# Kernel optimization log

Hardware: AMD Instinct MI355X
Metric: run time of the kernel (lower is better)

The kernel has to match this reference:

```python
import jax, jax.numpy as jnp
import numpy as np
import math

B, S, INP = 64, 512, 64
D, H, L, DFF, LAT = 512, 8, 2, 2048, 128
SPARSE = 0.1  # sparse_factor default used by TransformerEncoderLayer


def _ln(x, g, b, eps=1e-5):
    m = x.mean(-1, keepdims=True)
    v = ((x - m) ** 2).mean(-1, keepdims=True)
    return (x - m) / jnp.sqrt(v + eps) * g + b


def _pe(s, d):
    pos = jnp.arange(s, dtype=jnp.float32)[:, None]
    div = jnp.exp(jnp.arange(0, d, 2, dtype=jnp.float32) * (-math.log(10000.0) / d))
    pe = jnp.zeros((s, d), dtype=jnp.float32)
    return pe.at[:, 0::2].set(jnp.sin(pos * div)).at[:, 1::2].set(jnp.cos(pos * div))


def _attn(h, g1, b1, wq, wk, wv, woW, wob):
    # h: (S, B, d). Faithful to source: transpose(1,2) yields (S, H, B, dk),
    # so attention is computed ACROSS THE BATCH axis at each timestep.
    s, bb, d = h.shape
    dk = d // H
    res = h
    hn = _ln(h, g1, b1)
    to_heads = lambda w: (hn @ w).reshape(s, bb, H, dk).swapaxes(1, 2)  # (S,H,B,dk)
    q, k, v = to_heads(wq), to_heads(wk), to_heads(wv)
    scores = jnp.einsum('shbd,shcd->shbc', q, k) / math.sqrt(dk)  # (S,H,B,B)
    kk = max(1, int(bb * SPARSE))  # topk row-sparsify before softmax
    thresh = jax.lax.top_k(scores, kk)[0][..., -1:]
    scores = jnp.where(scores >= thresh, scores, -1e9)
    w = jax.nn.softmax(scores, axis=-1)
    ctx = jnp.einsum('shbc,shcd->shbd', w, v).swapaxes(1, 2).reshape(s, bb, d)
    return ctx @ woW + wob + res


def _encoder(x, inW, inb, p):
    # x: (B, S, in_dim) -> (B, S, D)
    h = jnp.swapaxes(x, 0, 1)  # (S, B, in)
    h = (h @ inW + inb) * math.sqrt(D)
    h = h + _pe(h.shape[0], D)[:, None, :]
    for l in range(L):
        h = _attn(h, p['g1'][l], p['b1'][l], p['wq'][l], p['wk'][l], p['wv'][l], p['woW'][l], p['wob'][l])
        res = h
        f = _ln(h, p['g2'][l], p['b2'][l])
        f = jax.nn.gelu(f @ p['f1W'][l] + p['f1b'][l], approximate=False)
        h = f @ p['f2W'][l] + p['f2b'][l] + res
    h = _ln(h, p['gf'], p['bf'])
    return jnp.swapaxes(h, 0, 1)


_PKEYS = ['g1', 'b1', 'wq', 'wk', 'wv', 'woW', 'wob', 'g2', 'b2', 'f1W', 'f1b', 'f2W', 'f2b', 'gf', 'bf']


def _forward(x, enc_in_W, enc_in_b, enc_g1, enc_b1, enc_wq, enc_wk, enc_wv, enc_woW, enc_wob,
             enc_g2, enc_b2, enc_f1W, enc_f1b, enc_f2W, enc_f2b, enc_gf, enc_bf,
             mu_W, mu_b, lv_W, lv_b, dec_in_W, dec_in_b, dec_g1, dec_b1, dec_wq, dec_wk, dec_wv,
             dec_woW, dec_wob, dec_g2, dec_b2, dec_f1W, dec_f1b, dec_f2W, dec_f2b, dec_gf, dec_bf,
             out_W, out_b):
    enc_p = dict(zip(_PKEYS, [enc_g1, enc_b1, enc_wq, enc_wk, enc_wv, enc_woW, enc_wob, enc_g2, enc_b2, enc_f1W, enc_f1b, enc_f2W, enc_f2b, enc_gf, enc_bf]))
    dec_p = dict(zip(_PKEYS, [dec_g1, dec_b1, dec_wq, dec_wk, dec_wv, dec_woW, dec_wob, dec_g2, dec_b2, dec_f1W, dec_f1b, dec_f2W, dec_f2b, dec_gf, dec_bf]))
    enc_out = _encoder(x, enc_in_W, enc_in_b, enc_p)  # (B,S,D)
    pooled = enc_out.mean(axis=1)                      # (B,D)
    mu = pooled @ mu_W + mu_b
    logvar = pooled @ lv_W + lv_b
    z = mu  # eval mode: no reparameterization sampling
    z_seq = jnp.broadcast_to(z[:, None, :], (z.shape[0], S, LAT))
    dec_out = _encoder(z_seq, dec_in_W, dec_in_b, dec_p)
    recon = dec_out @ out_W + out_b
    return recon, mu, logvar


def setup_inputs() -> dict:
    key = jax.random.key(0)
    ks = iter(jax.random.split(key, 64))
    n = lambda shape, s=0.02: jax.random.normal(next(ks), shape, dtype=jnp.float32) * s

    def stack_params():
        return dict(
            g1=jnp.ones((L, D)), b1=jnp.zeros((L, D)),
            wq=n((L, D, D)), wk=n((L, D, D)), wv=n((L, D, D)),
            woW=n((L, D, D)), wob=jnp.zeros((L, D)),
            g2=jnp.ones((L, D)), b2=jnp.zeros((L, D)),
            f1W=n((L, D, DFF)), f1b=jnp.zeros((L, DFF)),
            f2W=n((L, DFF, D)), f2b=jnp.zeros((L, D)),
            gf=jnp.ones((D,)), bf=jnp.zeros((D,)))

    inp = {
        'x': jax.random.normal(next(ks), (B, S, INP), dtype=jnp.float32),
        'enc_in_W': n((INP, D), 0.05), 'enc_in_b': jnp.zeros((D,)),
        'mu_W': n((D, LAT), 0.05), 'mu_b': jnp.zeros((LAT,)),
        'lv_W': n((D, LAT), 0.05), 'lv_b': jnp.zeros((LAT,)),
        'dec_in_W': n((LAT, D), 0.05), 'dec_in_b': jnp.zeros((D,)),
        'out_W': n((D, INP), 0.05), 'out_b': jnp.zeros((INP,)),
    }
    for k_, v in stack_params().items():
        inp['enc_' + k_] = v
    for k_, v in stack_params().items():
        inp['dec_' + k_] = v
    return inp


def reference(x, enc_in_W, enc_in_b, enc_g1, enc_b1, enc_wq, enc_wk, enc_wv, enc_woW, enc_wob,
              enc_g2, enc_b2, enc_f1W, enc_f1b, enc_f2W, enc_f2b, enc_gf, enc_bf,
              mu_W, mu_b, lv_W, lv_b, dec_in_W, dec_in_b, dec_g1, dec_b1, dec_wq, dec_wk, dec_wv,
              dec_woW, dec_wob, dec_g2, dec_b2, dec_f1W, dec_f1b, dec_f2W, dec_f2b, dec_gf, dec_bf,
              out_W, out_b):
    return _forward(x, enc_in_W, enc_in_b, enc_g1, enc_b1, enc_wq, enc_wk, enc_wv, enc_woW, enc_wob,
                    enc_g2, enc_b2, enc_f1W, enc_f1b, enc_f2W, enc_f2b, enc_gf, enc_bf,
                    mu_W, mu_b, lv_W, lv_b, dec_in_W, dec_in_b, dec_g1, dec_b1, dec_wq, dec_wk, dec_wv,
                    dec_woW, dec_wob, dec_g2, dec_b2, dec_f1W, dec_f1b, dec_f2W, dec_f2b, dec_gf, dec_bf,
                    out_W, out_b)
```

## Files before the change

kernel.cpp:

```cpp
#include <hip/hip_runtime.h>
#include <math.h>


#define SQRT_D 22.62741699796952f
#define PE_C   0.017988946039015984f

typedef short frag8 __attribute__((ext_vector_type(8)));
typedef float accf4 __attribute__((ext_vector_type(4)));

#define GLL16(g, l) __builtin_amdgcn_global_load_lds( \
    (const __attribute__((address_space(1))) void*)(g), \
    (__attribute__((address_space(3))) void*)(l), 16, 0, 0)

__device__ __forceinline__ float bf2f(unsigned short u) {
    union { unsigned i; float f; } v; v.i = ((unsigned)u) << 16; return v.f;
}
__device__ __forceinline__ unsigned short f2bf(float f) {
    union { float f; unsigned i; } v; v.f = f;
    unsigned r = v.i + 0x7fff + ((v.i >> 16) & 1);
    return (unsigned short)(r >> 16);
}
__device__ __forceinline__ float pe_val(int s, int d) {
    float div = expf(-(float)(d & ~1) * PE_C);
    float ang = (float)s * div;
    return (d & 1) ? cosf(ang) : sinf(ang);
}
__device__ __forceinline__ float gelu_exact(float x) {
    return 0.5f * x * (1.0f + erff(x * 0.7071067811865476f));
}
__device__ __forceinline__ float gelu_fast(float x) {
    float xs = x * 0.7071067811865476f;
    float ax = fabsf(xs);
    float t  = 1.0f / (1.0f + 0.3275911f * ax);
    float p  = t * (0.254829592f + t * (-0.284496736f + t * (1.421413741f +
               t * (-1.453152027f + t * 1.061405429f))));
    float er = 1.0f - p * __expf(-ax * ax);
    er = (xs < 0.0f) ? -er : er;
    return 0.5f * x * (1.0f + er);
}

__device__ __forceinline__ void phase_bar() {
    __builtin_amdgcn_sched_barrier(0);
    __builtin_amdgcn_s_barrier();
    __builtin_amdgcn_sched_barrier(0);
}

__global__ __launch_bounds__(256) void pe_k(float* __restrict__ pe)
{
    const int s = blockIdx.x;
    const int d = threadIdx.x;
    pe[s * 512 + d]       = pe_val(s, d);
    pe[s * 512 + d + 256] = pe_val(s, d + 256);
}

__global__ __launch_bounds__(256) void embed_gemm_k(
    const float* __restrict__ x, const float* __restrict__ W,
    const float* __restrict__ bias, const float* __restrict__ pe,
    float* __restrict__ h)
{
    __shared__ float As[64][68];
    __shared__ float Ws[64][68];
    const int s = blockIdx.y;
    const int col0 = blockIdx.x * 64;
    const int tid = threadIdx.x;
#pragma unroll
    for (int i = 0; i < 16; i++) {
        int idx = i * 256 + tid;
        int r = idx >> 6, kk = idx & 63;
        As[kk][r] = x[((size_t)r * 512 + s) * 64 + kk];
        Ws[r][kk] = W[(size_t)r * 512 + col0 + kk];
    }
    __syncthreads();
    const int tm = (tid >> 4) << 2;
    const int tn = (tid & 15) << 2;
    float acc[4][4] = {};
#pragma unroll 8
    for (int kk = 0; kk < 64; kk++) {
        float4 a4 = *reinterpret_cast<const float4*>(&As[kk][tm]);
        float4 b4 = *reinterpret_cast<const float4*>(&Ws[kk][tn]);
        const float a[4] = {a4.x, a4.y, a4.z, a4.w};
        const float b[4] = {b4.x, b4.y, b4.z, b4.w};
#pragma unroll
        for (int i = 0; i < 4; i++)
#pragma unroll
            for (int j = 0; j < 4; j++)
                acc[i][j] += a[i] * b[j];
    }
    const int c = col0 + tn;
    float4 bi = *reinterpret_cast<const float4*>(&bias[c]);
    float4 pp = *reinterpret_cast<const float4*>(&pe[s * 512 + c]);
#pragma unroll
    for (int i = 0; i < 4; i++) {
        size_t row = ((size_t)s * 64 + tm + i) * 512;
        float4 o;
        o.x = (acc[i][0] + bi.x) * SQRT_D + pp.x;
        o.y = (acc[i][1] + bi.y) * SQRT_D + pp.y;
        o.z = (acc[i][2] + bi.z) * SQRT_D + pp.z;
        o.w = (acc[i][3] + bi.w) * SQRT_D + pp.w;
        *reinterpret_cast<float4*>(&h[row + c]) = o;
    }
}

__global__ __launch_bounds__(256) void dec_embed_k(
    const float* __restrict__ zemb, const float* __restrict__ pe,
    float* __restrict__ h)
{
    const int i4 = (blockIdx.x * 256 + threadIdx.x) * 4;
    const int d = i4 & 511;
    const int t = i4 >> 9;
    const int s = t >> 6, b = t & 63;
    float4 z = *reinterpret_cast<const float4*>(&zemb[b * 512 + d]);
    float4 p = *reinterpret_cast<const float4*>(&pe[s * 512 + d]);
    float4 o;
    o.x = z.x * SQRT_D + p.x;
    o.y = z.y * SQRT_D + p.y;
    o.z = z.z * SQRT_D + p.z;
    o.w = z.w * SQRT_D + p.w;
    *reinterpret_cast<float4*>(&h[i4]) = o;
}

__global__ __launch_bounds__(256) void stats_k(
    const float* __restrict__ x, float* __restrict__ st)
{
    const int row = blockIdx.x;
    const int tid = threadIdx.x;
    const float* xr = x + (size_t)row * 512;
    float2 vv = *reinterpret_cast<const float2*>(&xr[tid * 2]);
    float v0 = vv.x, v1 = vv.y;
    float ssum = v0 + v1;
#pragma unroll
    for (int off = 32; off > 0; off >>= 1) ssum += __shfl_down(ssum, off, 64);
    __shared__ float red[4];
    __shared__ float red2[4];
    const int wid = tid >> 6, lane = tid & 63;
    if (lane == 0) red[wid] = ssum;
    __syncthreads();
    float m = (red[0] + red[1] + red[2] + red[3]) * (1.f / 512.f);
    float d0 = v0 - m, d1 = v1 - m;
    float s2 = d0 * d0 + d1 * d1;
#pragma unroll
    for (int off = 32; off > 0; off >>= 1) s2 += __shfl_down(s2, off, 64);
    if (lane == 0) red2[wid] = s2;
    __syncthreads();
    if (tid == 0) {
        float var = (red2[0] + red2[1] + red2[2] + red2[3]) * (1.f / 512.f);
        st[row * 2]     = m;
        st[row * 2 + 1] = rsqrtf(var + 1e-5f);
    }
}

__global__ __launch_bounds__(256) void cast_ln_k(
    const float* __restrict__ x, const float* __restrict__ g,
    const float* __restrict__ b, unsigned short* __restrict__ y)
{
    const int row = blockIdx.x;
    const int tid = threadIdx.x;
    const float* xr = x + (size_t)row * 512;
    float2 vv = *reinterpret_cast<const float2*>(&xr[tid * 2]);
    float v0 = vv.x, v1 = vv.y;
    float ssum = v0 + v1;
#pragma unroll
    for (int off = 32; off > 0; off >>= 1) ssum += __shfl_down(ssum, off, 64);
    __shared__ float red[4];
    __shared__ float red2[4];
    const int wid = tid >> 6, lane = tid & 63;
    if (lane == 0) red[wid] = ssum;
    __syncthreads();
    float m = (red[0] + red[1] + red[2] + red[3]) * (1.f / 512.f);
    float d0 = v0 - m, d1 = v1 - m;
    float s2 = d0 * d0 + d1 * d1;
#pragma unroll
    for (int off = 32; off > 0; off >>= 1) s2 += __shfl_down(s2, off, 64);
    if (lane == 0) red2[wid] = s2;
    __syncthreads();
    float var = (red2[0] + red2[1] + red2[2] + red2[3]) * (1.f / 512.f);
    float rstd = rsqrtf(var + 1e-5f);
    float2 gg = *reinterpret_cast<const float2*>(&g[tid * 2]);
    float2 bb = *reinterpret_cast<const float2*>(&b[tid * 2]);
    ushort2 o;
    o.x = f2bf(d0 * rstd * gg.x + bb.x);
    o.y = f2bf(d1 * rstd * gg.y + bb.y);
    *reinterpret_cast<ushort2*>(&y[(size_t)row * 512 + tid * 2]) = o;
}

struct WTDesc { const float* src; unsigned short* dst; int Kd; int Nd; };

__global__ __launch_bounds__(256) void wtcast6_k(
    WTDesc d0, WTDesc d1, WTDesc d2, WTDesc d3, WTDesc d4, WTDesc d5)
{
    WTDesc d;
    switch (blockIdx.z) {
        case 0: d = d0; break; case 1: d = d1; break; case 2: d = d2; break;
        case 3: d = d3; break; case 4: d = d4; break; default: d = d5; break;
    }
    const int n0 = blockIdx.x * 32, k0 = blockIdx.y * 32;
    if (n0 >= d.Nd || k0 >= d.Kd) return;
    __shared__ float t[32][33];
    const int tx = threadIdx.x & 31, ty = threadIdx.x >> 5;
#pragma unroll
    for (int i = 0; i < 32; i += 8)
        t[ty + i][tx] = d.src[(size_t)(k0 + ty + i) * d.Nd + (n0 + tx)];
    __syncthreads();
#pragma unroll
    for (int i = 0; i < 32; i += 8)
        d.dst[(size_t)(n0 + ty + i) * d.Kd + (k0 + tx)] = f2bf(t[tx][ty + i]);
}

template<int ACT, int OUTBF, int RES, int BIAS>
__global__ __launch_bounds__(256, 2) void mgemm128_k(
    const unsigned short* __restrict__ A, int lda,
    const unsigned short* __restrict__ Bt, int ldb,
    const float* __restrict__ bias,
    const float* res, float* Cf, unsigned short* Cb, int ldc, int K)
{
    __shared__ unsigned short sm[32768];
    const int tid = threadIdx.x;
    const int wave = tid >> 6, lane = tid & 63;

    int bx = blockIdx.x, by = blockIdx.y;
    if (gridDim.x == 256) {
        const int id = blockIdx.x + (blockIdx.y << 8);
        const int span = gridDim.y << 4;
        const int xcd = id & 7;
        const int q = id >> 3;
        const int hb = q / span;
        const int r2 = q - hb * span;
        bx = (xcd << 5) + (hb << 4) + (r2 & 15);
        by = r2 >> 4;
    }
    const int row0 = bx * 128;
    const int col0 = by * 128;

    const int wr = wave >> 1, wc = wave & 1;
    const int wrbase = wr * 64, wcbase = wc * 64;
    const int frow = lane & 15;
    const int fcol = (lane >> 4) * 8;
    const int fxorE = (lane & 7) << 3;
    const int ccol = ((lane & 7) ^ (lane >> 3)) * 8;

    const int NT = K >> 6;

    auto stageA = [&](int buf, int k0t) {
#pragma unroll
        for (int i = 0; i < 4; i++) {
            int chunk = wave * 4 + i;
            GLL16(A + (size_t)(row0 + chunk * 8 + (lane >> 3)) * lda + k0t + ccol,
                  &sm[buf * 16384 + chunk * 512]);
        }
    };
    auto stageB = [&](int buf, int k0t) {
#pragma unroll
        for (int i = 0; i < 4; i++) {
            int chunk = wave * 4 + i;
            GLL16(Bt + (size_t)(col0 + chunk * 8 + (lane >> 3)) * ldb + k0t + ccol,
                  &sm[buf * 16384 + 8192 + chunk * 512]);
        }
    };

    accf4 acc[4][4] = {};
    frag8 af[4][2], bfr[4][2];

    stageA(0, 0); stageB(0, 0);
    if (NT > 1) { stageA(1, 64); stageB(1, 64); }
    if (NT > 1) asm volatile("s_waitcnt vmcnt(8)" ::: "memory");
    else        asm volatile("s_waitcnt vmcnt(0)" ::: "memory");
    phase_bar();

    for (int t = 0; t < NT; ++t) {
        const int ab = (t & 1) * 16384;
        const int bb = ab + 8192;
        const bool pf = (t + 2) < NT;
        const int kpf = (t + 2) << 6;

#pragma unroll
        for (int mi = 0; mi < 4; mi++)
#pragma unroll
            for (int ks = 0; ks < 2; ks++)
                af[mi][ks] = *(const frag8*)&sm[ab + (wrbase + mi * 16 + frow) * 64 + ((ks * 32 + fcol) ^ fxorE)];
#pragma unroll
        for (int nj = 0; nj < 4; nj++)
#pragma unroll
            for (int ks = 0; ks < 2; ks++)
                bfr[nj][ks] = *(const frag8*)&sm[bb + (wcbase + nj * 16 + frow) * 64 + ((ks * 32 + fcol) ^ fxorE)];
        asm volatile("s_waitcnt lgkmcnt(0)" ::: "memory");
        phase_bar();

        if (pf) { stageB(t & 1, kpf); stageA(t & 1, kpf); }
        __builtin_amdgcn_s_setprio(1);
#pragma unroll
        for (int mi = 0; mi < 4; mi++)
#pragma unroll
            for (int nj = 0; nj < 4; nj++)
#pragma unroll
                for (int ks = 0; ks < 2; ks++)
                    acc[mi][nj] = __builtin_amdgcn_mfma_f32_16x16x32_bf16(
                        bfr[nj][ks], af[mi][ks], acc[mi][nj], 0, 0, 0);
        __builtin_amdgcn_s_setprio(0);
        if (pf) asm volatile("s_waitcnt vmcnt(8)" ::: "memory");
        else    asm volatile("s_waitcnt vmcnt(0)" ::: "memory");
        phase_bar();
    }

    const int lrow = lane & 15;
    const int lcol = (lane >> 4) * 4;
#pragma unroll
    for (int mi = 0; mi < 4; mi++) {
        const int r = row0 + wrbase + mi * 16 + lrow;
#pragma unroll
        for (int nj = 0; nj < 4; nj++) {
            const int c = col0 + wcbase + nj * 16 + lcol;
            float4 v = make_float4(acc[mi][nj][0], acc[mi][nj][1],
                                   acc[mi][nj][2], acc[mi][nj][3]);
            if (BIAS) {
                float4 bi = *reinterpret_cast<const float4*>(&bias[c]);
                v.x += bi.x; v.y += bi.y; v.z += bi.z; v.w += bi.w;
            }
            if (ACT) {
                v.x = gelu_fast(v.x); v.y = gelu_fast(v.y);
                v.z = gelu_fast(v.z); v.w = gelu_fast(v.w);
            }
            if (RES) {
                float4 rr = *reinterpret_cast<const float4*>(&res[(size_t)r * ldc + c]);
                v.x += rr.x; v.y += rr.y; v.z += rr.z; v.w += rr.w;
            }
            if (OUTBF) {
                ushort4 o;
                o.x = f2bf(v.x); o.y = f2bf(v.y); o.z = f2bf(v.z); o.w = f2bf(v.w);
                *reinterpret_cast<ushort4*>(&Cb[(size_t)r * ldc + c]) = o;
            } else {
                *reinterpret_cast<float4*>(&Cf[(size_t)r * ldc + c]) = v;
            }
        }
    }
}

__global__ __launch_bounds__(256) void attn3_k(
    const unsigned short* __restrict__ qkv, unsigned short* __restrict__ ctx)
{
    __shared__ unsigned short QL[4096];
    __shared__ unsigned short KL[4096];
    __shared__ unsigned short VT[4096];
    __shared__ float ScT[64][68];
    __shared__ float dsums[64][4];
    __shared__ float rds[64];
    const int blk = blockIdx.x;
    const int sl = blk >> 3, hh = blk & 7;
    const int tid = threadIdx.x;
    const int wave = tid >> 6, lane = tid & 63;
    const size_t qbase = (size_t)sl * 64 * 1536 + (size_t)hh * 64;

    {
        const int r = tid >> 2;
        const int dg = (tid & 3) << 4;
        const int x = (r & 7) << 3;
        const unsigned short* gp = qkv + qbase + (size_t)r * 1536 + dg;
        frag8 q0 = *(const frag8*)(gp);
        frag8 q1 = *(const frag8*)(gp + 8);
        frag8 k0 = *(const frag8*)(gp + 512);
        frag8 k1 = *(const frag8*)(gp + 520);
        frag8 v0 = *(const frag8*)(gp + 1024);
        frag8 v1 = *(const frag8*)(gp + 1032);
        *(frag8*)&QL[r * 64 + (dg ^ x)]       = q0;
        *(frag8*)&QL[r * 64 + ((dg + 8) ^ x)] = q1;
        *(frag8*)&KL[r * 64 + (dg ^ x)]       = k0;
        *(frag8*)&KL[r * 64 + ((dg + 8) ^ x)] = k1;
#pragma unroll
        for (int i = 0; i < 16; i++) {
            int ii = (i + r) & 15;
            int j = dg + ii;
            unsigned short e = (unsigned short)(ii < 8 ? v0[ii] : v1[ii - 8]);
            VT[j * 64 + (r ^ ((j & 7) << 3))] = e;
        }
    }
    __syncthreads();

    const int frow = lane & 15;
    const int fcol8 = (lane >> 4) * 8;
    const int fx = (lane & 7) << 3;

    {
        const int c0 = wave * 16;
        accf4 sacc[4] = {};
#pragma unroll
        for (int ks = 0; ks < 2; ks++) {
            frag8 kf = *(const frag8*)&KL[(c0 + frow) * 64 + ((ks * 32 + fcol8) ^ fx)];
#pragma unroll
            for (int rt = 0; rt < 4; rt++) {
                frag8 qf = *(const frag8*)&QL[(rt * 16 + frow) * 64 + ((ks * 32 + fcol8) ^ fx)];
                sacc[rt] = __builtin_amdgcn_mfma_f32_16x16x32_bf16(
                    qf, kf, sacc[rt], 0, 0, 0);
            }
        }
        const int cc = c0 + frow;
        const int rb = (lane >> 4) * 4;
#pragma unroll
        for (int rt = 0; rt < 4; rt++) {
            float4 s4;
            s4.x = sacc[rt][0] * 0.125f; s4.y = sacc[rt][1] * 0.125f;
            s4.z = sacc[rt][2] * 0.125f; s4.w = sacc[rt][3] * 0.125f;
            *(float4*)&ScT[cc][rt * 16 + rb] = s4;
        }
    }
    __syncthreads();

    const int row = tid & 63, seg = tid >> 6;
    float* candp = (float*)&KL[0];
    {
        float top[6];
#pragma unroll
        for (int i = 0; i < 6; i++) top[i] = -3.4e38f;
#pragma unroll
        for (int c = seg * 16; c < seg * 16 + 16; c++) {
            float vv = ScT[c][row];
            if (vv > top[5]) {
                top[5] = vv;
#pragma unroll
                for (int i = 5; i > 0; i--)
                    if (top[i] > top[i - 1]) { float t = top[i]; top[i] = top[i - 1]; top[i - 1] = t; }
            }
        }
#pragma unroll
        for (int i = 0; i < 6; i++) candp[row * 24 + seg * 6 + i] = top[i];
    }
    __syncthreads();
    if (seg == 0) {
        float t6[6];
#pragma unroll
        for (int i = 0; i < 6; i++) t6[i] = -3.4e38f;
#pragma unroll
        for (int j = 0; j < 24; j++) {
            float vv = candp[row * 24 + j];
            if (vv > t6[5]) {
                t6[5] = vv;
#pragma unroll
                for (int i = 5; i > 0; i--)
                    if (t6[i] > t6[i - 1]) { float t = t6[i]; t6[i] = t6[i - 1]; t6[i - 1] = t; }
            }
        }
        ScT[row][64] = t6[5];
        ScT[row][65] = t6[0];
    }
    __syncthreads();
    {
        const float thresh = ScT[row][64], mx = ScT[row][65];
        const int xr = (row & 7) << 3;
        float dsum = 0.f;
#pragma unroll
        for (int c = seg * 16; c < seg * 16 + 16; c++) {
            float vv = ScT[c][row];
            float w = (vv >= thresh) ? expf(vv - mx) : 0.f;
            unsigned short wb = f2bf(w);
            dsum += bf2f(wb);
            QL[row * 64 + (c ^ xr)] = wb;
        }
        dsums[row][seg] = dsum;
    }
    __syncthreads();
    if (tid < 64)
        rds[tid] = 1.f / (dsums[tid][0] + dsums[tid][1] + dsums[tid][2] + dsums[tid][3]);
    __syncthreads();

    {
        const int r0 = wave * 16;
        accf4 pacc[4] = {};
#pragma unroll
        for (int ks = 0; ks < 2; ks++) {
            frag8 pf = *(const frag8*)&QL[(r0 + frow) * 64 + ((ks * 32 + fcol8) ^ fx)];
#pragma unroll
            for (int jt = 0; jt < 4; jt++) {
                frag8 vf = *(const frag8*)&VT[(jt * 16 + frow) * 64 + ((ks * 32 + fcol8) ^ fx)];
                pacc[jt] = __builtin_amdgcn_mfma_f32_16x16x32_bf16(
                    vf, pf, pacc[jt], 0, 0, 0);
            }
        }
        const int rr = r0 + frow;
        const int jb = (lane >> 4) * 4;
        const float sc = rds[rr];
#pragma unroll
        for (int jt = 0; jt < 4; jt++) {
            ushort4 o;
            o.x = f2bf(pacc[jt][0] * sc); o.y = f2bf(pacc[jt][1] * sc);
            o.z = f2bf(pacc[jt][2] * sc); o.w = f2bf(pacc[jt][3] * sc);
            *reinterpret_cast<ushort4*>(
                &ctx[(size_t)(sl * 64 + rr) * 512 + hh * 64 + jt * 16 + jb]) = o;
        }
    }
}

template<int ACT, int PERM, int LN>
__global__ __launch_bounds__(256) void gemm_k(
    const float* __restrict__ A, int lda,
    const float* __restrict__ W, int ldw,
    const float* __restrict__ bias,
    const float* res,
    float* C, int ldc,
    int K,
    const float* __restrict__ stats,
    const float* __restrict__ lng, const float* __restrict__ lnb)
{
    __shared__ float As[16][68];
    __shared__ float Ws[16][68];
    __shared__ float ms[64], rss[64];
    const int row0 = blockIdx.y * 64;
    const int col0 = blockIdx.x * 64;
    const int tid = threadIdx.x;
    if (LN) {
        if (tid < 64) {
            ms[tid]  = stats[(row0 + tid) * 2];
            rss[tid] = stats[(row0 + tid) * 2 + 1];
        }
        __syncthreads();
    }
    const int tm = (tid >> 4) << 2;
    const int tn = (tid & 15) << 2;
    float acc[4][4] = {};
    for (int k0 = 0; k0 < K; k0 += 16) {
#pragma unroll
        for (int i = 0; i < 4; i++) {
            int idx = i * 256 + tid;
            int r = idx >> 4, kk = idx & 15;
            float v = A[(size_t)(row0 + r) * lda + (k0 + kk)];
            if (LN) v = (v - ms[r]) * rss[r] * lng[k0 + kk] + lnb[k0 + kk];
            As[kk][r] = v;
        }
#pragma unroll
        for (int i = 0; i < 4; i++) {
            int idx = i * 256 + tid;
            int kk = idx >> 6, c = idx & 63;
            Ws[kk][c] = W[(size_t)(k0 + kk) * ldw + (col0 + c)];
        }
        __syncthreads();
#pragma unroll
        for (int kk = 0; kk < 16; kk++) {
            float4 a4 = *reinterpret_cast<const float4*>(&As[kk][tm]);
            float4 b4 = *reinterpret_cast<const float4*>(&Ws[kk][tn]);
            const float a[4] = {a4.x, a4.y, a4.z, a4.w};
            const float b[4] = {b4.x, b4.y, b4.z, b4.w};
#pragma unroll
            for (int i = 0; i < 4; i++)
#pragma unroll
                for (int j = 0; j < 4; j++)
                    acc[i][j] += a[i] * b[j];
        }
        __syncthreads();
    }
#pragma unroll
    for (int i = 0; i < 4; i++) {
        int r = row0 + tm + i;
#pragma unroll
        for (int j = 0; j < 4; j++) {
            int c = col0 + tn + j;
            float v = acc[i][j];
            if (bias) v += bias[c];
            if (ACT == 1) v = gelu_exact(v);
            if (res) v += res[(size_t)r * ldc + c];
            if (PERM) {
                int bb = r & 63, ss = r >> 6;
                C[((size_t)bb * 512 + ss) * ldc + c] = v;
            } else {
                C[(size_t)r * ldc + c] = v;
            }
        }
    }
}

__global__ __launch_bounds__(512) void pool_ln_k(
    const float* __restrict__ h, const float* __restrict__ st,
    const float* __restrict__ gf, const float* __restrict__ bf,
    float* __restrict__ pooled)
{
    const int b = blockIdx.x;
    const int d = threadIdx.x;
    const float g = gf[d], bb = bf[d];
    float acc = 0.f;
    for (int s = 0; s < 512; s++) {
        int r = s * 64 + b;
        float m = st[r * 2], rs = st[r * 2 + 1];
        acc += (h[(size_t)r * 512 + d] - m) * rs * g + bb;
    }
    pooled[b * 512 + d] = acc * (1.f / 512.f);
}

static void run_layer2(const float* const* p, int l,
                       float* h, unsigned short* hn_bf,
                       unsigned short* qkv, int chunk_rows,
                       unsigned short* f1c, int cw,
                       unsigned short* wqkv_t, unsigned short* wo_t,
                       unsigned short* f1_t, unsigned short* f2_t,
                       hipStream_t stream)
{
    const float* g1  = p[0] + l * 512;
    const float* b1  = p[1] + l * 512;
    const float* wq  = p[2] + (size_t)l * 262144;
    const float* wk  = p[3] + (size_t)l * 262144;
    const float* wv  = p[4] + (size_t)l * 262144;
    const float* wo  = p[5] + (size_t)l * 262144;
    const float* wob = p[6] + l * 512;
    const float* g2  = p[7] + l * 512;
    const float* b2  = p[8] + l * 512;
    const float* f1W = p[9] + (size_t)l * 1048576;
    const float* f1b = p[10] + l * 2048;
    const float* f2W = p[11] + (size_t)l * 1048576;
    const float* f2b = p[12] + l * 512;

    {
        WTDesc d0 = {wq,  wqkv_t,          512,  512};
        WTDesc d1 = {wk,  wqkv_t + 262144, 512,  512};
        WTDesc d2 = {wv,  wqkv_t + 524288, 512,  512};
        WTDesc d3 = {wo,  wo_t,            512,  512};
        WTDesc d4 = {f1W, f1_t,            512,  2048};
        WTDesc d5 = {f2W, f2_t,            2048, 512};
        wtcast6_k<<<dim3(64, 64, 6), 256, 0, stream>>>(d0, d1, d2, d3, d4, d5);
    }

    cast_ln_k<<<32768, 256, 0, stream>>>(h, g1, b1, hn_bf);
    for (int r0 = 0; r0 < 32768; r0 += chunk_rows) {
        mgemm128_k<0, 1, 0, 0><<<dim3(chunk_rows / 128, 12), 256, 0, stream>>>(
            hn_bf + (size_t)r0 * 512, 512, wqkv_t, 512, nullptr,
            nullptr, nullptr, qkv, 1536, 512);
        attn3_k<<<(chunk_rows / 64) * 8, 256, 0, stream>>>(
            qkv, hn_bf + (size_t)r0 * 512);
    }
    mgemm128_k<0, 0, 1, 1><<<dim3(256, 4), 256, 0, stream>>>(
        hn_bf, 512, wo_t, 512, wob, h, h, nullptr, 512, 512);

    cast_ln_k<<<32768, 256, 0, stream>>>(h, g2, b2, hn_bf);
    for (int c0 = 0; c0 < 2048; c0 += cw) {
        mgemm128_k<1, 1, 0, 1><<<dim3(256, cw / 128), 256, 0, stream>>>(
            hn_bf, 512, f1_t + (size_t)c0 * 512, 512, f1b + c0,
            nullptr, nullptr, f1c, cw, 512);
        if (c0 == 0)
            mgemm128_k<0, 0, 1, 1><<<dim3(256, 4), 256, 0, stream>>>(
                f1c, cw, f2_t + c0, 2048, f2b, h, h, nullptr, 512, cw);
        else
            mgemm128_k<0, 0, 1, 0><<<dim3(256, 4), 256, 0, stream>>>(
                f1c, cw, f2_t + c0, 2048, nullptr, h, h, nullptr, 512, cw);
    }
}

extern "C" void kernel_launch(void* const* d_in, const int* in_sizes, int n_in,
                              void* d_out, int out_size, void* d_ws, size_t ws_size,
                              hipStream_t stream)
{
    const float* x       = (const float*)d_in[0];
    const float* enc_inW = (const float*)d_in[1];
    const float* enc_inb = (const float*)d_in[2];
    const float* mu_W    = (const float*)d_in[3];
    const float* mu_b    = (const float*)d_in[4];
    const float* lv_W    = (const float*)d_in[5];
    const float* lv_b    = (const float*)d_in[6];
    const float* dec_inW = (const float*)d_in[7];
    const float* dec_inb = (const float*)d_in[8];
    const float* out_W   = (const float*)d_in[9];
    const float* out_b   = (const float*)d_in[10];
    const float* const* ep = (const float* const*)(d_in + 11);
    const float* const* dp = (const float* const*)(d_in + 26);

    float* fout   = (float*)d_out;
    float* mu_out = fout + 2097152;
    float* lv_out = mu_out + 8192;

    const size_t SZ = (size_t)32768 * 512;
    size_t off = 0;
    char* base = (char*)d_ws;
    auto take = [&](size_t bytes) -> char* {
        char* pp = base + off;
        off = (off + bytes + 255) & ~(size_t)255;
        return pp;
    };
    float*          h      = (float*)take(SZ * 4);
    unsigned short* hn_bf  = (unsigned short*)take(SZ * 2);
    unsigned short* wqkv_t = (unsigned short*)take(1536 * 512 * 2);
    unsigned short* wo_t   = (unsigned short*)take(512 * 512 * 2);
    unsigned short* f1_t   = (unsigned short*)take(2048 * 512 * 2);
    unsigned short* f2_t   = (unsigned short*)take(512 * 2048 * 2);
    float*          stats  = (float*)take(65536 * 4);
    float*          pooled = (float*)take(131072);
    float*          zemb   = (float*)take(131072);
    float*          pe     = (float*)take(512 * 512 * 4);

    unsigned short* qkv; unsigned short* f1c;
    int chunk_rows, cw;
    size_t rem = (ws_size > off) ? (ws_size - off) : 0;
    const size_t F1_FULL  = (size_t)32768 * 2048 * 2;
    const size_t QKV_FULL = (size_t)32768 * 1536 * 2;
    if (rem >= F1_FULL + 512) {
        unsigned short* share = (unsigned short*)take(F1_FULL);
        qkv = share; f1c = share; chunk_rows = 32768; cw = 2048;
    } else if (rem >= QKV_FULL + 512) {
        unsigned short* share = (unsigned short*)take(QKV_FULL);
        qkv = share; f1c = share; chunk_rows = 32768; cw = 512;
    } else if (rem >= (size_t)32768 * 512 * 2 + 512) {
        unsigned short* share = (unsigned short*)take((size_t)32768 * 512 * 2);
        qkv = share; f1c = share; chunk_rows = 8192; cw = 512;
    } else {
        qkv = (unsigned short*)take((size_t)4096 * 1536 * 2);
        chunk_rows = 4096;
        f1c = (unsigned short*)fout; cw = 128;
    }

    const int M = 32768;

    pe_k<<<512, 256, 0, stream>>>(pe);

    embed_gemm_k<<<dim3(8, 512), 256, 0, stream>>>(x, enc_inW, enc_inb, pe, h);
    for (int l = 0; l < 2; l++)
        run_layer2(ep, l, h, hn_bf, qkv, chunk_rows, f1c, cw,
                   wqkv_t, wo_t, f1_t, f2_t, stream);

    stats_k<<<M, 256, 0, stream>>>(h, stats);
    pool_ln_k<<<64, 512, 0, stream>>>(h, stats, ep[13], ep[14], pooled);
    gemm_k<0, 0, 0><<<dim3(2, 1), 256, 0, stream>>>(pooled, 512, mu_W, 128, mu_b,
                                                    nullptr, mu_out, 128, 512,
                                                    nullptr, nullptr, nullptr);
    gemm_k<0, 0, 0><<<dim3(2, 1), 256, 0, stream>>>(pooled, 512, lv_W, 128, lv_b,
                                                    nullptr, lv_out, 128, 512,
                                                    nullptr, nullptr, nullptr);
    gemm_k<0, 0, 0><<<dim3(8, 1), 256, 0, stream>>>(mu_out, 128, dec_inW, 512, dec_inb,
                                                    nullptr, zemb, 512, 128,
                                                    nullptr, nullptr, nullptr);
    dec_embed_k<<<16384, 256, 0, stream>>>(zemb, pe, h);

    for (int l = 0; l < 2; l++)
        run_layer2(dp, l, h, hn_bf, qkv, chunk_rows, f1c, cw,
                   wqkv_t, wo_t, f1_t, f2_t, stream);

    stats_k<<<M, 256, 0, stream>>>(h, stats);
    gemm_k<0, 1, 1><<<dim3(1, M / 64), 256, 0, stream>>>(
        h, 512, out_W, 64, out_b, nullptr, fout, 64, 512, stats, dp[13], dp[14]);
}
```

Before: 2.042 ms.

## Add 256x256-tile GEMM kernel with 4-stage LDS pipeline for encoder layers

```diff
diff --git a/kernel.cpp b/kernel.cpp
--- a/kernel.cpp
+++ b/kernel.cpp
@@ -207,6 +207,135 @@
 }
 
 template<int ACT, int OUTBF, int RES, int BIAS>
+__global__ __launch_bounds__(512, 2) void mgemm256r_k(
+    const unsigned short* __restrict__ A, int lda,
+    const unsigned short* __restrict__ Bt, int ldb,
+    const float* __restrict__ bias,
+    const float* res, float* Cf, unsigned short* Cb, int ldc, int K)
+{
+    __shared__ unsigned short sm[65536];
+    const int tid = threadIdx.x;
+    const int wave = tid >> 6, lane = tid & 63;
+
+    const int gx = gridDim.x, gy = gridDim.y;
+    const int id = blockIdx.x + blockIdx.y * gx;
+    const int nwg = gx * gy;
+    const int lid = (id & 7) * (nwg >> 3) + (id >> 3);
+    const int row0 = (lid / gy) * 256;
+    const int col0 = (lid % gy) * 256;
+
+    const int wr = wave >> 2, wc = wave & 3;
+    const int wrbase = wr * 128, wcbase = wc * 64;
+
+    const int frow = lane & 15, c0 = (lane >> 4) * 8;
+    int offA[8], offB[4];
+#pragma unroll
+    for (int mi = 0; mi < 8; mi++) {
+        int row = wrbase + mi * 16 + frow, pr = row >> 1;
+        offA[mi] = pr * 64 + ((((row & 1) * 32) + c0) ^ ((pr & 7) << 3));
+    }
+#pragma unroll
+    for (int nj = 0; nj < 4; nj++) {
+        int row = wcbase + nj * 16 + frow, pr = row >> 1;
+        offB[nj] = 8192 + pr * 64 + ((((row & 1) * 32) + c0) ^ ((pr & 7) << 3));
+    }
+
+    const int chunk = wave * 2;
+    const int w8 = ((lane & 7) ^ (lane >> 3)) << 3;
+    const int sb = w8 >> 5, sc = w8 & 31;
+    const int pr0 = chunk * 8 + (lane >> 3);
+    const int pr1 = pr0 + 8;
+    const unsigned short* gA0 = A  + (size_t)(row0 + pr0 * 2 + sb) * lda + sc;
+    const unsigned short* gA1 = A  + (size_t)(row0 + pr1 * 2 + sb) * lda + sc;
+    const unsigned short* gB0 = Bt + (size_t)(col0 + pr0 * 2 + sb) * ldb + sc;
+    const unsigned short* gB1 = Bt + (size_t)(col0 + pr1 * 2 + sb) * ldb + sc;
+    const int dA0 = chunk * 512, dA1 = dA0 + 512;
+    const int dB0 = 8192 + dA0,  dB1 = dB0 + 512;
+
+    const int NT = K >> 5;
+    accf4 acc[8][4] = {};
+    frag8 fA[8], fB0[4], fB1[4];
+
+#define STAGE(kt) do { const int _b = ((kt) & 3) << 14; const int _k = (kt) << 5; \
+    GLL16(gA0 + _k, &sm[_b + dA0]); GLL16(gA1 + _k, &sm[_b + dA1]);              \
+    GLL16(gB0 + _k, &sm[_b + dB0]); GLL16(gB1 + _k, &sm[_b + dB1]); } while (0)
+
+#define PHASE(T, BCUR, BNXT) do {                                               \
+    const bool pf3 = (T) + 3 < NT;                                              \
+    const bool pf1 = (T) + 1 < NT;                                              \
+    if (pf3) STAGE((T) + 3);                                                    \
+    const int rb = (((T) + 1) & 3) << 14;                                       \
+    if (pf1) {                                                                  \
+        _Pragma("unroll")                                                       \
+        for (int nj = 0; nj < 4; nj++)                                          \
+            BNXT[nj] = *(const frag8*)&sm[rb + offB[nj]];                       \
+    }                                                                           \
+    __builtin_amdgcn_s_setprio(1);                                              \
+    _Pragma("unroll")                                                           \
+    for (int mi = 0; mi < 8; mi++) {                                            \
+        frag8 a = fA[mi];                                                       \
+        _Pragma("unroll")                                                       \
+        for (int nj = 0; nj < 4; nj++)                                          \
+            acc[mi][nj] = __builtin_amdgcn_mfma_f32_16x16x32_bf16(              \
+                BCUR[nj], a, acc[mi][nj], 0, 0, 0);                             \
+        if (pf1) fA[mi] = *(const frag8*)&sm[rb + offA[mi]];                    \
+    }                                                                           \
+    __builtin_amdgcn_s_setprio(0);                                              \
+    asm volatile("s_waitcnt lgkmcnt(0)" ::: "memory");                          \
+    if (pf3) asm volatile("s_waitcnt vmcnt(4)" ::: "memory");                   \
+    else     asm volatile("s_waitcnt vmcnt(0)" ::: "memory");                   \
+    phase_bar();                                                                \
+} while (0)
+
+    STAGE(0); STAGE(1); STAGE(2);
+    asm volatile("s_waitcnt vmcnt(4)" ::: "memory");
+    phase_bar();
+#pragma unroll
+    for (int mi = 0; mi < 8; mi++) fA[mi] = *(const frag8*)&sm[offA[mi]];
+#pragma unroll
+    for (int nj = 0; nj < 4; nj++) fB0[nj] = *(const frag8*)&sm[offB[nj]];
+
+    for (int t = 0; t < NT; t += 2) {
+        PHASE(t,     fB0, fB1);
+        PHASE(t + 1, fB1, fB0);
+    }
+#undef PHASE
+#undef STAGE
+
+    const int lrow = lane & 15;
+    const int lcol = (lane >> 4) * 4;
+#pragma unroll
+    for (int mi = 0; mi < 8; mi++) {
+        const int r = row0 + wrbase + mi * 16 + lrow;
+#pragma unroll
+        for (int nj = 0; nj < 4; nj++) {
+            const int c = col0 + wcbase + nj * 16 + lcol;
+            float4 v = make_float4(acc[mi][nj][0], acc[mi][nj][1],
+                                   acc[mi][nj][2], acc[mi][nj][3]);
+            if (BIAS) {
+                float4 bi = *reinterpret_cast<const float4*>(&bias[c]);
+                v.x += bi.x; v.y += bi.y; v.z += bi.z; v.w += bi.w;
+            }
+            if (ACT) {
+                v.x = gelu_fast(v.x); v.y = gelu_fast(v.y);
+                v.z = gelu_fast(v.z); v.w = gelu_fast(v.w);
+            }
+            if (RES) {
+                float4 rr = *reinterpret_cast<const float4*>(&res[(size_t)r * ldc + c]);
+                v.x += rr.x; v.y += rr.y; v.z += rr.z; v.w += rr.w;
+            }
+            if (OUTBF) {
+                ushort4 o;
+                o.x = f2bf(v.x); o.y = f2bf(v.y); o.z = f2bf(v.z); o.w = f2bf(v.w);
+                *reinterpret_cast<ushort4*>(&Cb[(size_t)r * ldc + c]) = o;
+            } else {
+                *reinterpret_cast<float4*>(&Cf[(size_t)r * ldc + c]) = v;
+            }
+        }
+    }
+}
+
+template<int ACT, int OUTBF, int RES, int BIAS>
 __global__ __launch_bounds__(256, 2) void mgemm128_k(
     const unsigned short* __restrict__ A, int lda,
     const unsigned short* __restrict__ Bt, int ldb,
@@ -216,28 +345,14 @@
     __shared__ unsigned short sm[32768];
     const int tid = threadIdx.x;
     const int wave = tid >> 6, lane = tid & 63;
-
-    int bx = blockIdx.x, by = blockIdx.y;
-    if (gridDim.x == 256) {
-        const int id = blockIdx.x + (blockIdx.y << 8);
-        const int span = gridDim.y << 4;
-        const int xcd = id & 7;
-        const int q = id >> 3;
-        const int hb = q / span;
-        const int r2 = q - hb * span;
-        bx = (xcd << 5) + (hb << 4) + (r2 & 15);
-        by = r2 >> 4;
-    }
-    const int row0 = bx * 128;
-    const int col0 = by * 128;
-
+    const int row0 = blockIdx.x * 128;
+    const int col0 = blockIdx.y * 128;
     const int wr = wave >> 1, wc = wave & 1;
     const int wrbase = wr * 64, wcbase = wc * 64;
     const int frow = lane & 15;
     const int fcol = (lane >> 4) * 8;
     const int fxorE = (lane & 7) << 3;
     const int ccol = ((lane & 7) ^ (lane >> 3)) * 8;
-
     const int NT = K >> 6;
 
     auto stageA = [&](int buf, int k0t) {
@@ -259,7 +374,6 @@
 
     accf4 acc[4][4] = {};
     frag8 af[4][2], bfr[4][2];
-
     stageA(0, 0); stageB(0, 0);
     if (NT > 1) { stageA(1, 64); stageB(1, 64); }
     if (NT > 1) asm volatile("s_waitcnt vmcnt(8)" ::: "memory");
@@ -271,7 +385,6 @@
         const int bb = ab + 8192;
         const bool pf = (t + 2) < NT;
         const int kpf = (t + 2) << 6;
-
 #pragma unroll
         for (int mi = 0; mi < 4; mi++)
 #pragma unroll
@@ -284,7 +397,6 @@
                 bfr[nj][ks] = *(const frag8*)&sm[bb + (wcbase + nj * 16 + frow) * 64 + ((ks * 32 + fcol) ^ fxorE)];
         asm volatile("s_waitcnt lgkmcnt(0)" ::: "memory");
         phase_bar();
-
         if (pf) { stageB(t & 1, kpf); stageA(t & 1, kpf); }
         __builtin_amdgcn_s_setprio(1);
 #pragma unroll
@@ -615,26 +727,40 @@
 
     cast_ln_k<<<32768, 256, 0, stream>>>(h, g1, b1, hn_bf);
     for (int r0 = 0; r0 < 32768; r0 += chunk_rows) {
-        mgemm128_k<0, 1, 0, 0><<<dim3(chunk_rows / 128, 12), 256, 0, stream>>>(
+        mgemm256r_k<0, 1, 0, 0><<<dim3(chunk_rows / 256, 6), 512, 0, stream>>>(
             hn_bf + (size_t)r0 * 512, 512, wqkv_t, 512, nullptr,
             nullptr, nullptr, qkv, 1536, 512);
         attn3_k<<<(chunk_rows / 64) * 8, 256, 0, stream>>>(
             qkv, hn_bf + (size_t)r0 * 512);
     }
-    mgemm128_k<0, 0, 1, 1><<<dim3(256, 4), 256, 0, stream>>>(
+    mgemm256r_k<0, 0, 1, 1><<<dim3(128, 2), 512, 0, stream>>>(
         hn_bf, 512, wo_t, 512, wob, h, h, nullptr, 512, 512);
 
     cast_ln_k<<<32768, 256, 0, stream>>>(h, g2, b2, hn_bf);
-    for (int c0 = 0; c0 < 2048; c0 += cw) {
-        mgemm128_k<1, 1, 0, 1><<<dim3(256, cw / 128), 256, 0, stream>>>(
-            hn_bf, 512, f1_t + (size_t)c0 * 512, 512, f1b + c0,
-            nullptr, nullptr, f1c, cw, 512);
-        if (c0 == 0)
-            mgemm128_k<0, 0, 1, 1><<<dim3(256, 4), 256, 0, stream>>>(
-                f1c, cw, f2_t + c0, 2048, f2b, h, h, nullptr, 512, cw);
-        else
-            mgemm128_k<0, 0, 1, 0><<<dim3(256, 4), 256, 0, stream>>>(
-                f1c, cw, f2_t + c0, 2048, nullptr, h, h, nullptr, 512, cw);
+    if (cw >= 256) {
+        for (int c0 = 0; c0 < 2048; c0 += cw) {
+            mgemm256r_k<1, 1, 0, 1><<<dim3(128, cw / 256), 512, 0, stream>>>(
+                hn_bf, 512, f1_t + (size_t)c0 * 512, 512, f1b + c0,
+                nullptr, nullptr, f1c, cw, 512);
+            if (c0 == 0)
+                mgemm256r_k<0, 0, 1, 1><<<dim3(128, 2), 512, 0, stream>>>(
+                    f1c, cw, f2_t + c0, 2048, f2b, h, h, nullptr, 512, cw);
+            else
+                mgemm256r_k<0, 0, 1, 0><<<dim3(128, 2), 512, 0, stream>>>(
+                    f1c, cw, f2_t + c0, 2048, nullptr, h, h, nullptr, 512, cw);
+        }
+    } else {
+        for (int c0 = 0; c0 < 2048; c0 += cw) {
+            mgemm128_k<1, 1, 0, 1><<<dim3(256, cw / 128), 256, 0, stream>>>(
+                hn_bf, 512, f1_t + (size_t)c0 * 512, 512, f1b + c0,
+                nullptr, nullptr, f1c, cw, 512);
+            if (c0 == 0)
+                mgemm128_k<0, 0, 1, 1><<<dim3(256, 4), 256, 0, stream>>>(
+                    f1c, cw, f2_t + c0, 2048, f2b, h, h, nullptr, 512, cw);
+            else
+                mgemm128_k<0, 0, 1, 0><<<dim3(256, 4), 256, 0, stream>>>(
+                    f1c, cw, f2_t + c0, 2048, nullptr, h, h, nullptr, 512, cw);
+        }
     }
 }
 
```

Measured after the change: 2.077 ms. About the same (+1.7%).

## Replace double-buffered 128x128 GEMM with B-resident 128x64 tile and direct A loads

Applied to the files above, without the earlier changes.

```diff
diff --git a/kernel.cpp b/kernel.cpp
--- a/kernel.cpp
+++ b/kernel.cpp
@@ -37,12 +37,6 @@
     float er = 1.0f - p * __expf(-ax * ax);
     er = (xs < 0.0f) ? -er : er;
     return 0.5f * x * (1.0f + er);
-}
-
-__device__ __forceinline__ void phase_bar() {
-    __builtin_amdgcn_sched_barrier(0);
-    __builtin_amdgcn_s_barrier();
-    __builtin_amdgcn_sched_barrier(0);
 }
 
 __global__ __launch_bounds__(256) void pe_k(float* __restrict__ pe)
@@ -207,108 +201,103 @@
 }
 
 template<int ACT, int OUTBF, int RES, int BIAS>
-__global__ __launch_bounds__(256, 2) void mgemm128_k(
+__global__ __launch_bounds__(256, 2) void sgemm_k(
     const unsigned short* __restrict__ A, int lda,
     const unsigned short* __restrict__ Bt, int ldb,
     const float* __restrict__ bias,
     const float* res, float* Cf, unsigned short* Cb, int ldc, int K)
 {
-    __shared__ unsigned short sm[32768];
+    __shared__ unsigned short Bs[64 * 512];
     const int tid = threadIdx.x;
     const int wave = tid >> 6, lane = tid & 63;
 
-    int bx = blockIdx.x, by = blockIdx.y;
-    if (gridDim.x == 256) {
-        const int id = blockIdx.x + (blockIdx.y << 8);
-        const int span = gridDim.y << 4;
-        const int xcd = id & 7;
-        const int q = id >> 3;
-        const int hb = q / span;
-        const int r2 = q - hb * span;
-        bx = (xcd << 5) + (hb << 4) + (r2 & 15);
-        by = r2 >> 4;
-    }
-    const int row0 = bx * 128;
-    const int col0 = by * 128;
-
-    const int wr = wave >> 1, wc = wave & 1;
-    const int wrbase = wr * 64, wcbase = wc * 64;
+    const int gy = gridDim.y;
+    const int nwg = gridDim.x * gy;
+    const int id = blockIdx.x * gy + blockIdx.y;
+    const int lid = (id & 7) * (nwg >> 3) + (id >> 3);
+    const int row0 = (lid / gy) * 128;
+    const int col0 = (lid % gy) * 64;
+
     const int frow = lane & 15;
-    const int fcol = (lane >> 4) * 8;
-    const int fxorE = (lane & 7) << 3;
-    const int ccol = ((lane & 7) ^ (lane >> 3)) * 8;
-
-    const int NT = K >> 6;
-
-    auto stageA = [&](int buf, int k0t) {
-#pragma unroll
-        for (int i = 0; i < 4; i++) {
-            int chunk = wave * 4 + i;
-            GLL16(A + (size_t)(row0 + chunk * 8 + (lane >> 3)) * lda + k0t + ccol,
-                  &sm[buf * 16384 + chunk * 512]);
-        }
-    };
-    auto stageB = [&](int buf, int k0t) {
-#pragma unroll
-        for (int i = 0; i < 4; i++) {
-            int chunk = wave * 4 + i;
-            GLL16(Bt + (size_t)(col0 + chunk * 8 + (lane >> 3)) * ldb + k0t + ccol,
-                  &sm[buf * 16384 + 8192 + chunk * 512]);
-        }
-    };
-
-    accf4 acc[4][4] = {};
-    frag8 af[4][2], bfr[4][2];
-
-    stageA(0, 0); stageB(0, 0);
-    if (NT > 1) { stageA(1, 64); stageB(1, 64); }
-    if (NT > 1) asm volatile("s_waitcnt vmcnt(8)" ::: "memory");
-    else        asm volatile("s_waitcnt vmcnt(0)" ::: "memory");
-    phase_bar();
-
-    for (int t = 0; t < NT; ++t) {
-        const int ab = (t & 1) * 16384;
-        const int bb = ab + 8192;
-        const bool pf = (t + 2) < NT;
-        const int kpf = (t + 2) << 6;
-
-#pragma unroll
-        for (int mi = 0; mi < 4; mi++)
-#pragma unroll
-            for (int ks = 0; ks < 2; ks++)
-                af[mi][ks] = *(const frag8*)&sm[ab + (wrbase + mi * 16 + frow) * 64 + ((ks * 32 + fcol) ^ fxorE)];
-#pragma unroll
-        for (int nj = 0; nj < 4; nj++)
-#pragma unroll
-            for (int ks = 0; ks < 2; ks++)
-                bfr[nj][ks] = *(const frag8*)&sm[bb + (wcbase + nj * 16 + frow) * 64 + ((ks * 32 + fcol) ^ fxorE)];
-        asm volatile("s_waitcnt lgkmcnt(0)" ::: "memory");
-        phase_bar();
-
-        if (pf) { stageB(t & 1, kpf); stageA(t & 1, kpf); }
-        __builtin_amdgcn_s_setprio(1);
-#pragma unroll
-        for (int mi = 0; mi < 4; mi++)
-#pragma unroll
-            for (int nj = 0; nj < 4; nj++)
-#pragma unroll
-                for (int ks = 0; ks < 2; ks++)
-                    acc[mi][nj] = __builtin_amdgcn_mfma_f32_16x16x32_bf16(
-                        bfr[nj][ks], af[mi][ks], acc[mi][nj], 0, 0, 0);
-        __builtin_amdgcn_s_setprio(0);
-        if (pf) asm volatile("s_waitcnt vmcnt(8)" ::: "memory");
-        else    asm volatile("s_waitcnt vmcnt(0)" ::: "memory");
-        phase_bar();
-    }
-
-    const int lrow = lane & 15;
+    const int fk8  = (lane >> 4) * 8;
+    const int r0 = row0 + wave * 32;
+
+    const int KC  = (K < 512) ? K : 512;
+    const int NTC = KC >> 5;
+
+    accf4 acc[2][4] = {};
+
+    for (int kc = 0; kc < K; kc += KC) {
+        if (kc) __syncthreads();
+        if (KC == 512) {
+#pragma unroll
+            for (int i = 0; i < 16; i++) {
+                int rowb = wave * 16 + i;
+                GLL16(Bt + (size_t)(col0 + rowb) * ldb + kc
+                          + ((lane * 8) ^ ((rowb & 7) << 3)),
+                      &Bs[rowb * 512]);
+            }
+            asm volatile("s_waitcnt vmcnt(0)" ::: "memory");
+        } else {
+            for (int idx = tid; idx < 64 * (KC >> 3); idx += 256) {
+                int rowb = idx / (KC >> 3), c8 = (idx % (KC >> 3)) * 8;
+                frag8 v = *(const frag8*)&Bt[(size_t)(col0 + rowb) * ldb + kc + c8];
+                *(frag8*)&Bs[rowb * 512 + (c8 ^ ((rowb & 7) << 3))] = v;
+            }
+        }
+        __syncthreads();
+
+        const unsigned short* Ab = A + (size_t)(r0 + frow) * lda + kc + fk8;
+        const int ldr = 16 * lda;
+
+        frag8 a0A = *(const frag8*)(Ab);
+        frag8 a0B = *(const frag8*)(Ab + ldr);
+        frag8 a1A = *(const frag8*)(Ab + 32);
+        frag8 a1B = *(const frag8*)(Ab + ldr + 32);
+
+        for (int kt = 0; kt < NTC; kt += 2) {
+            {
+                const int kb = kt * 32 + fk8;
+#pragma unroll
+                for (int nj = 0; nj < 4; nj++) {
+                    const int rowb = nj * 16 + frow;
+                    frag8 bf = *(const frag8*)&Bs[rowb * 512 + (kb ^ ((rowb & 7) << 3))];
+                    acc[0][nj] = __builtin_amdgcn_mfma_f32_16x16x32_bf16(
+                        bf, a0A, acc[0][nj], 0, 0, 0);
+                    acc[1][nj] = __builtin_amdgcn_mfma_f32_16x16x32_bf16(
+                        bf, a0B, acc[1][nj], 0, 0, 0);
+                }
+            }
+            if (kt + 2 < NTC) {
+                a0A = *(const frag8*)(Ab + (kt + 2) * 32);
+                a0B = *(const frag8*)(Ab + ldr + (kt + 2) * 32);
+            }
+            {
+                const int kb = (kt + 1) * 32 + fk8;
+#pragma unroll
+                for (int nj = 0; nj < 4; nj++) {
+                    const int rowb = nj * 16 + frow;
+                    frag8 bf = *(const frag8*)&Bs[rowb * 512 + (kb ^ ((rowb & 7) << 3))];
+                    acc[0][nj] = __builtin_amdgcn_mfma_f32_16x16x32_bf16(
+                        bf, a1A, acc[0][nj], 0, 0, 0);
+                    acc[1][nj] = __builtin_amdgcn_mfma_f32_16x16x32_bf16(
+                        bf, a1B, acc[1][nj], 0, 0, 0);
+                }
+            }
+            if (kt + 3 < NTC) {
+                a1A = *(const frag8*)(Ab + (kt + 3) * 32);
+                a1B = *(const frag8*)(Ab + ldr + (kt + 3) * 32);
+            }
+        }
+    }
+
     const int lcol = (lane >> 4) * 4;
 #pragma unroll
-    for (int mi = 0; mi < 4; mi++) {
-        const int r = row0 + wrbase + mi * 16 + lrow;
+    for (int mi = 0; mi < 2; mi++) {
+        const int r = r0 + mi * 16 + frow;
 #pragma unroll
         for (int nj = 0; nj < 4; nj++) {
-            const int c = col0 + wcbase + nj * 16 + lcol;
+            const int c = col0 + nj * 16 + lcol;
             float4 v = make_float4(acc[mi][nj][0], acc[mi][nj][1],
                                    acc[mi][nj][2], acc[mi][nj][3]);
             if (BIAS) {
@@ -615,25 +604,25 @@
 
     cast_ln_k<<<32768, 256, 0, stream>>>(h, g1, b1, hn_bf);
     for (int r0 = 0; r0 < 32768; r0 += chunk_rows) {
-        mgemm128_k<0, 1, 0, 0><<<dim3(chunk_rows / 128, 12), 256, 0, stream>>>(
+        sgemm_k<0, 1, 0, 0><<<dim3(chunk_rows / 128, 24), 256, 0, stream>>>(
             hn_bf + (size_t)r0 * 512, 512, wqkv_t, 512, nullptr,
             nullptr, nullptr, qkv, 1536, 512);
         attn3_k<<<(chunk_rows / 64) * 8, 256, 0, stream>>>(
             qkv, hn_bf + (size_t)r0 * 512);
     }
-    mgemm128_k<0, 0, 1, 1><<<dim3(256, 4), 256, 0, stream>>>(
+    sgemm_k<0, 0, 1, 1><<<dim3(256, 8), 256, 0, stream>>>(
         hn_bf, 512, wo_t, 512, wob, h, h, nullptr, 512, 512);
 
     cast_ln_k<<<32768, 256, 0, stream>>>(h, g2, b2, hn_bf);
     for (int c0 = 0; c0 < 2048; c0 += cw) {
-        mgemm128_k<1, 1, 0, 1><<<dim3(256, cw / 128), 256, 0, stream>>>(
+        sgemm_k<1, 1, 0, 1><<<dim3(256, cw / 64), 256, 0, stream>>>(
             hn_bf, 512, f1_t + (size_t)c0 * 512, 512, f1b + c0,
             nullptr, nullptr, f1c, cw, 512);
         if (c0 == 0)
-            mgemm128_k<0, 0, 1, 1><<<dim3(256, 4), 256, 0, stream>>>(
+            sgemm_k<0, 0, 1, 1><<<dim3(256, 8), 256, 0, stream>>>(
                 f1c, cw, f2_t + c0, 2048, f2b, h, h, nullptr, 512, cw);
         else
-            mgemm128_k<0, 0, 1, 0><<<dim3(256, 4), 256, 0, stream>>>(
+            sgemm_k<0, 0, 1, 0><<<dim3(256, 8), 256, 0, stream>>>(
                 f1c, cw, f2_t + c0, 2048, nullptr, h, h, nullptr, 512, cw);
     }
 }
```

After: 3.227 ms. 58.1% more time.

## Split GEMM k-step into two MFMA phases and drop XCD block remapping

Applied to the files above, without the earlier changes.

```diff
diff --git a/kernel.cpp b/kernel.cpp
--- a/kernel.cpp
+++ b/kernel.cpp
@@ -216,21 +216,8 @@
     __shared__ unsigned short sm[32768];
     const int tid = threadIdx.x;
     const int wave = tid >> 6, lane = tid & 63;
-
-    int bx = blockIdx.x, by = blockIdx.y;
-    if (gridDim.x == 256) {
-        const int id = blockIdx.x + (blockIdx.y << 8);
-        const int span = gridDim.y << 4;
-        const int xcd = id & 7;
-        const int q = id >> 3;
-        const int hb = q / span;
-        const int r2 = q - hb * span;
-        bx = (xcd << 5) + (hb << 4) + (r2 & 15);
-        by = r2 >> 4;
-    }
-    const int row0 = bx * 128;
-    const int col0 = by * 128;
-
+    const int row0 = blockIdx.x * 128;
+    const int col0 = blockIdx.y * 128;
     const int wr = wave >> 1, wc = wave & 1;
     const int wrbase = wr * 64, wcbase = wc * 64;
     const int frow = lane & 15;
@@ -258,7 +245,7 @@
     };
 
     accf4 acc[4][4] = {};
-    frag8 af[4][2], bfr[4][2];
+    frag8 af0[4], af1[4], bfr[4][2];
 
     stageA(0, 0); stageB(0, 0);
     if (NT > 1) { stageA(1, 64); stageB(1, 64); }
@@ -274,28 +261,37 @@
 
 #pragma unroll
         for (int mi = 0; mi < 4; mi++)
-#pragma unroll
-            for (int ks = 0; ks < 2; ks++)
-                af[mi][ks] = *(const frag8*)&sm[ab + (wrbase + mi * 16 + frow) * 64 + ((ks * 32 + fcol) ^ fxorE)];
+            af0[mi] = *(const frag8*)&sm[ab + (wrbase + mi * 16 + frow) * 64 + (fcol ^ fxorE)];
 #pragma unroll
         for (int nj = 0; nj < 4; nj++)
 #pragma unroll
             for (int ks = 0; ks < 2; ks++)
                 bfr[nj][ks] = *(const frag8*)&sm[bb + (wcbase + nj * 16 + frow) * 64 + ((ks * 32 + fcol) ^ fxorE)];
-        asm volatile("s_waitcnt lgkmcnt(0)" ::: "memory");
         phase_bar();
-
-        if (pf) { stageB(t & 1, kpf); stageA(t & 1, kpf); }
         __builtin_amdgcn_s_setprio(1);
 #pragma unroll
         for (int mi = 0; mi < 4; mi++)
 #pragma unroll
             for (int nj = 0; nj < 4; nj++)
-#pragma unroll
-                for (int ks = 0; ks < 2; ks++)
-                    acc[mi][nj] = __builtin_amdgcn_mfma_f32_16x16x32_bf16(
-                        bfr[nj][ks], af[mi][ks], acc[mi][nj], 0, 0, 0);
+                acc[mi][nj] = __builtin_amdgcn_mfma_f32_16x16x32_bf16(
+                    bfr[nj][0], af0[mi], acc[mi][nj], 0, 0, 0);
         __builtin_amdgcn_s_setprio(0);
+        phase_bar();
+
+#pragma unroll
+        for (int mi = 0; mi < 4; mi++)
+            af1[mi] = *(const frag8*)&sm[ab + (wrbase + mi * 16 + frow) * 64 + ((32 + fcol) ^ fxorE)];
+        if (pf) stageB(t & 1, kpf);
+        phase_bar();
+        __builtin_amdgcn_s_setprio(1);
+#pragma unroll
+        for (int mi = 0; mi < 4; mi++)
+#pragma unroll
+            for (int nj = 0; nj < 4; nj++)
+                acc[mi][nj] = __builtin_amdgcn_mfma_f32_16x16x32_bf16(
+                    bfr[nj][1], af1[mi], acc[mi][nj], 0, 0, 0);
+        __builtin_amdgcn_s_setprio(0);
+        if (pf) stageA(t & 1, kpf);
         if (pf) asm volatile("s_waitcnt vmcnt(8)" ::: "memory");
         else    asm volatile("s_waitcnt vmcnt(0)" ::: "memory");
         phase_bar();
```

Measured after the change: 2.202 ms. 1.08x slower.
